# Performance work log

Measured on AMD Instinct MI355X. Metric: run time of the kernel, lower is better.

## Reference

```python
import jax, jax.numpy as jnp
import numpy as np

B, T, I, H, C = 2048, 1024, 6, 38, 8


def setup_inputs() -> dict:
    key = jax.random.key(0)
    ks = jax.random.split(key, 9)
    s = 1.0 / np.sqrt(H)  # PyTorch LSTM init scale
    return {
        "x": jax.random.normal(ks[0], (B, T, I), dtype=jnp.float32),
        "Wih0": jax.random.normal(ks[1], (4 * H, I), dtype=jnp.float32) * s,
        "Whh0": jax.random.normal(ks[2], (4 * H, H), dtype=jnp.float32) * s,
        "b0": jax.random.normal(ks[3], (4 * H,), dtype=jnp.float32) * s,
        "Wih1": jax.random.normal(ks[4], (4 * H, H), dtype=jnp.float32) * s,
        "Whh1": jax.random.normal(ks[5], (4 * H, H), dtype=jnp.float32) * s,
        "b1": jax.random.normal(ks[6], (4 * H,), dtype=jnp.float32) * s,
        "Wc": jax.random.normal(ks[7], (C, H), dtype=jnp.float32) * s,
        "bc": jax.random.normal(ks[8], (C,), dtype=jnp.float32) * s,
    }


def _lstm_layer(x, Wih, Whh, b):
    # x: [B, T, I]; PyTorch gate order: i, f, g, o; combined bias b = b_ih + b_hh
    Bsz = x.shape[0]
    Hh = Whh.shape[1]
    gx = jnp.einsum('bti,gi->btg', x, Wih) + b  # [B, T, 4H], input projection batched

    def step(carry, g_t):
        h, c = carry
        g = g_t + h @ Whh.T  # [B, 4H]
        i, f, gg, o = jnp.split(g, 4, axis=-1)
        i = jax.nn.sigmoid(i)
        f = jax.nn.sigmoid(f)
        gg = jnp.tanh(gg)
        o = jax.nn.sigmoid(o)
        c = f * c + i * gg
        h = o * jnp.tanh(c)
        return (h, c), h

    h0 = jnp.zeros((Bsz, Hh), dtype=x.dtype)
    c0 = jnp.zeros((Bsz, Hh), dtype=x.dtype)
    _, hs = jax.lax.scan(step, (h0, c0), jnp.swapaxes(gx, 0, 1))  # hs: [T, B, H]
    return jnp.swapaxes(hs, 0, 1)  # [B, T, H]


def reference(x, Wih0, Whh0, b0, Wih1, Whh1, b1, Wc, bc):
    # 2-layer LSTM (dropout is identity at inference), classify last timestep hidden
    h1 = _lstm_layer(x, Wih0, Whh0, b0)
    h2 = _lstm_layer(h1, Wih1, Whh1, b1)
    last = h2[:, -1, :]  # [B, H]
    return last @ Wc.T + bc  # [B, C]
```

## Files before the change

kernel.cpp:

```cpp
#include <hip/hip_runtime.h>

#define TT    1024
#define BATCH 2048
#define NI    6
#define NH    38
#define NG    152
#define NCLS  8
#define NB    8
#define BLK   640
#define KP1   68
#define KP2   100
#define XK    40
#define H2K   48

typedef _Float16 f16;
typedef _Float16 f16x4 __attribute__((ext_vector_type(4)));
typedef _Float16 f16x8 __attribute__((ext_vector_type(8)));
typedef float    f32x4 __attribute__((ext_vector_type(4)));

__device__ __forceinline__ float fsig(float v)  { return __fdividef(1.0f, 1.0f + __expf(-v)); }
__device__ __forceinline__ float ftanh(float v) { return 1.0f - __fdividef(2.0f, 1.0f + __expf(2.0f*v)); }

__device__ __forceinline__ float wget1(const float* Wih0, const float* Whh0, int r, int k) {
    if (r >= NG) return 0.0f;
    const int u = r >> 2, g = r & 3;
    if (k < NH) return Whh0[(size_t)(g*NH + u)*NH + k];
    if (k >= XK && k < XK + NI) return Wih0[(size_t)(g*NH + u)*NI + (k - XK)];
    return 0.0f;
}
__device__ __forceinline__ float wget2(const float* Wih1, const float* Whh1, int r, int k) {
    if (r >= NG) return 0.0f;
    const int u = r >> 2, g = r & 3;
    if (k < NH) return Wih1[(size_t)(g*NH + u)*NH + k];
    if (k >= H2K && k < H2K + NH) return Whh1[(size_t)(g*NH + u)*NH + (k - H2K)];
    return 0.0f;
}

__device__ __forceinline__ f16x8 ldA1(const float* Wih0, const float* Whh0,
                                      int Tg, int F, int m16, int qq) {
    f16x8 r;
    #pragma unroll
    for (int e = 0; e < 8; ++e) {
        const int kk = 32*F + ((e < 4) ? (qq*4 + e) : (16 + qq*4 + e - 4));
        r[e] = (f16)wget1(Wih0, Whh0, 16*Tg + m16, kk);
    }
    return r;
}
__device__ __forceinline__ f16x8 ldA2(const float* Wih1, const float* Whh1,
                                      int Tg, int F, int m16, int qq) {
    f16x8 r;
    #pragma unroll
    for (int e = 0; e < 8; ++e) {
        const int kk = 32*F + ((e < 4) ? (qq*4 + e) : (16 + qq*4 + e - 4));
        r[e] = (f16)wget2(Wih1, Whh1, 16*Tg + m16, kk);
    }
    return r;
}

__device__ __forceinline__ f16x8 ldB(const f16* rb, int off) {
    const f16x4 lo = *(const f16x4*)(rb + off);
    const f16x4 hi = *(const f16x4*)(rb + off + 16);
    f16x8 r;
    r[0]=lo[0]; r[1]=lo[1]; r[2]=lo[2]; r[3]=lo[3];
    r[4]=hi[0]; r[5]=hi[1]; r[6]=hi[2]; r[7]=hi[3];
    return r;
}

#define MFMA16(A, B, C) __builtin_amdgcn_mfma_f32_16x16x32_f16(A, B, C, 0, 0, 0)

#define PWCORE(A, CREG) \
    const float ig = fsig((A)[0] + bsv0), fg = fsig((A)[1] + bsv1); \
    const float gg = ftanh((A)[2] + bsv2), og = fsig((A)[3] + bsv3); \
    const float cc = fg * (CREG) + ig * gg; (CREG) = cc; \
    const f16 hv = (f16)(og * ftanh(cc));


__global__ __launch_bounds__(BLK, 1) void lstm2_kernel(
    const float* __restrict__ x,
    const float* __restrict__ Wih0, const float* __restrict__ Whh0, const float* __restrict__ b0,
    const float* __restrict__ Wih1, const float* __restrict__ Whh1, const float* __restrict__ b1,
    const float* __restrict__ Wc,   const float* __restrict__ bc,
    float* __restrict__ out)
{
    __shared__ __align__(16) f16 l1buf[2][16][KP1];
    __shared__ __align__(16) f16 l2buf[2][16][KP2];
    __shared__ float ldspad[19456];

    const int tid   = threadIdx.x;
    const int bbase = blockIdx.x * NB;
    const int wid   = tid >> 6, lane = tid & 63;
    const int n     = lane & 15, qq = lane >> 4;

    if (bc[0] > 3.0e38f) ldspad[tid] = x[tid];

    {
        int* p1 = (int*)&l1buf[0][0][0];
        for (int idx = tid; idx < 2*16*KP1/2; idx += BLK) p1[idx] = 0;
        int* p2 = (int*)&l2buf[0][0][0];
        for (int idx = tid; idx < 2*16*KP2/2; idx += BLK) p2[idx] = 0;
    }
    __syncthreads();
    if (tid < NB * NI) {
        const int b = tid / NI, j = tid % NI;
        l1buf[1][b][XK + j] = (f16)x[(size_t)(bbase + b)*TT*NI + j];
    }

    const bool isL1 = (wid < 5);
    const int  T0   = 2 * (isL1 ? wid : wid - 5);
    const int  u0   = 4*T0 + qq, u1 = u0 + 4;
    const bool wen0 = (u0 < NH) && (n < NB);
    const bool wen1 = (u1 < NH) && (n < NB);

    f16x8 w00, w01, w02, w10, w11, w12;
    float bs00=0.f,bs01=0.f,bs02=0.f,bs03=0.f, bs10=0.f,bs11=0.f,bs12=0.f,bs13=0.f;
    {
        f16x8 z8; 
        #pragma unroll
        for (int e = 0; e < 8; ++e) z8[e] = (f16)0;
        w02 = z8; w12 = z8;
        if (isL1) {
            w00 = ldA1(Wih0, Whh0, T0,   0, n, qq);
            w01 = ldA1(Wih0, Whh0, T0,   1, n, qq);
            w10 = ldA1(Wih0, Whh0, T0+1, 0, n, qq);
            w11 = ldA1(Wih0, Whh0, T0+1, 1, n, qq);
            if (u0 < NH) { bs00=b0[u0]; bs01=b0[NH+u0]; bs02=b0[2*NH+u0]; bs03=b0[3*NH+u0]; }
            if (u1 < NH) { bs10=b0[u1]; bs11=b0[NH+u1]; bs12=b0[2*NH+u1]; bs13=b0[3*NH+u1]; }
        } else {
            w00 = ldA2(Wih1, Whh1, T0,   0, n, qq);
            w01 = ldA2(Wih1, Whh1, T0,   1, n, qq);
            w02 = ldA2(Wih1, Whh1, T0,   2, n, qq);
            w10 = ldA2(Wih1, Whh1, T0+1, 0, n, qq);
            w11 = ldA2(Wih1, Whh1, T0+1, 1, n, qq);
            w12 = ldA2(Wih1, Whh1, T0+1, 2, n, qq);
            if (u0 < NH) { bs00=b1[u0]; bs01=b1[NH+u0]; bs02=b1[2*NH+u0]; bs03=b1[3*NH+u0]; }
            if (u1 < NH) { bs10=b1[u1]; bs11=b1[NH+u1]; bs12=b1[2*NH+u1]; bs13=b1[3*NH+u1]; }
        }
    }

    const bool isPF = (tid < NB * NI);
    const float* xptr = nullptr;
    f16 *pfw0 = nullptr, *pfw1 = nullptr;
    if (isPF) {
        const int b = tid / NI, j = tid % NI;
        xptr = x + (size_t)(bbase + b)*TT*NI + NI + j;
        pfw0 = &l1buf[0][b][XK + j];
        pfw1 = &l1buf[1][b][XK + j];
    }

    float c0 = 0.0f, c1 = 0.0f;

    __syncthreads();

    #pragma unroll 1
    for (int i = 0; i <= TT; ++i) {
        const int s = i & 1, rs = s ^ 1;

        float xv = 0.0f;
        const bool pf = isPF && (i + 1 < TT);
        if (pf) xv = *xptr;

        if (isL1) {
            if (i < TT) {
                const f16* rb = &l1buf[rs][n][0];
                const f16x8 B0 = ldB(rb, 4*qq);
                const f16x8 B1 = ldB(rb, 32 + 4*qq);
                f32x4 a0 = {0.f,0.f,0.f,0.f}, a1 = {0.f,0.f,0.f,0.f};
                a0 = MFMA16(w00, B0, a0);
                a0 = MFMA16(w01, B1, a0);
                a1 = MFMA16(w10, B0, a1);
                a1 = MFMA16(w11, B1, a1);
                {
                    const float bsv0=bs00, bsv1=bs01, bsv2=bs02, bsv3=bs03;
                    PWCORE(a0, c0)
                    if (wen0) { l1buf[s][n][u0] = hv; l2buf[s][n][u0] = hv; }
                }
                {
                    const float bsv0=bs10, bsv1=bs11, bsv2=bs12, bsv3=bs13;
                    PWCORE(a1, c1)
                    if (wen1) { l1buf[s][n][u1] = hv; l2buf[s][n][u1] = hv; }
                }
            }
        } else {
            if (i >= 1) {
                const f16* rb = &l2buf[rs][n][0];
                const f16x8 B0 = ldB(rb, 4*qq);
                const f16x8 B1 = ldB(rb, 32 + 4*qq);
                const f16x8 B2 = ldB(rb, 64 + 4*qq);
                f32x4 a0 = {0.f,0.f,0.f,0.f}, a1 = {0.f,0.f,0.f,0.f};
                a0 = MFMA16(w00, B0, a0);
                a0 = MFMA16(w01, B1, a0);
                a0 = MFMA16(w02, B2, a0);
                a1 = MFMA16(w10, B0, a1);
                a1 = MFMA16(w11, B1, a1);
                a1 = MFMA16(w12, B2, a1);
                {
                    const float bsv0=bs00, bsv1=bs01, bsv2=bs02, bsv3=bs03;
                    PWCORE(a0, c0)
                    if (wen0) l2buf[s][n][H2K + u0] = hv;
                }
                {
                    const float bsv0=bs10, bsv1=bs11, bsv2=bs12, bsv3=bs13;
                    PWCORE(a1, c1)
                    if (wen1) l2buf[s][n][H2K + u1] = hv;
                }
            }
        }

        if (pf) { *(s ? pfw1 : pfw0) = (f16)xv; xptr += NI; }
        __syncthreads();
    }

    if (tid < NB * NCLS) {
        const int b = tid >> 3, c = tid & 7;
        float a = bc[c];
        #pragma unroll
        for (int k = 0; k < NH; ++k)
            a += Wc[c*NH + k] * (float)l2buf[0][b][H2K + k];
        out[(size_t)(bbase + b)*NCLS + c] = a;
    }
    if (bc[0] > 3.0e38f) out[tid] = ldspad[BLK - tid];
}

extern "C" void kernel_launch(void* const* d_in, const int* in_sizes, int n_in,
                              void* d_out, int out_size, void* d_ws, size_t ws_size,
                              hipStream_t stream) {
    const float* x    = (const float*)d_in[0];
    const float* Wih0 = (const float*)d_in[1];
    const float* Whh0 = (const float*)d_in[2];
    const float* b0   = (const float*)d_in[3];
    const float* Wih1 = (const float*)d_in[4];
    const float* Whh1 = (const float*)d_in[5];
    const float* b1   = (const float*)d_in[6];
    const float* Wc   = (const float*)d_in[7];
    const float* bc   = (const float*)d_in[8];
    float* out = (float*)d_out;

    dim3 grid(BATCH / NB);
    dim3 block(BLK);
    hipLaunchKernelGGL(lstm2_kernel, grid, block, 0, stream,
                       x, Wih0, Whh0, b0, Wih1, Whh1, b1, Wc, bc, out);
}
```

Baseline: 1.277 ms.

## Unify LSTM layer buffers, batch x prefetch via LDS ring, use LDS-only barrier

Merges the layer-1 and layer-2 hidden-state buffers into one shared buffer, so layer-1 lanes write each hidden value once instead of twice. The per-step global load of x is replaced by a batched load of 8 timesteps into registers, which are staged through a 16-deep LDS ring. This lets the per-step barrier wait only on LDS counters (lgkmcnt) rather than on outstanding global loads. The risk is in ring and index timing: layer 2 now reads its input from the same slot layer 1 writes to, and the x ring must stay in sync with the double buffer.

```diff
diff --git a/kernel.cpp b/kernel.cpp
--- a/kernel.cpp
+++ b/kernel.cpp
@@ -8,10 +8,10 @@
 #define NCLS  8
 #define NB    8
 #define BLK   640
-#define KP1   68
-#define KP2   100
+#define UK    100
 #define XK    40
 #define H2K   48
+#define RD    16
 
 typedef _Float16 f16;
 typedef _Float16 f16x4 __attribute__((ext_vector_type(4)));
@@ -74,6 +74,11 @@
     const float cc = fg * (CREG) + ig * gg; (CREG) = cc; \
     const f16 hv = (f16)(og * ftanh(cc));
 
+#define LBAR() \
+    asm volatile("s_waitcnt lgkmcnt(0)" ::: "memory"); \
+    __builtin_amdgcn_s_barrier(); \
+    asm volatile("" ::: "memory"); \
+    __builtin_amdgcn_sched_barrier(0);
 
 __global__ __launch_bounds__(BLK, 1) void lstm2_kernel(
     const float* __restrict__ x,
@@ -82,9 +87,9 @@
     const float* __restrict__ Wc,   const float* __restrict__ bc,
     float* __restrict__ out)
 {
-    __shared__ __align__(16) f16 l1buf[2][16][KP1];
-    __shared__ __align__(16) f16 l2buf[2][16][KP2];
-    __shared__ float ldspad[19456];
+    __shared__ __align__(16) f16 ubuf[2][16][UK];
+    __shared__ __align__(16) f16 xring[RD][48];
+    __shared__ float ldspad[20160];
 
     const int tid   = threadIdx.x;
     const int bbase = blockIdx.x * NB;
@@ -94,16 +99,10 @@
     if (bc[0] > 3.0e38f) ldspad[tid] = x[tid];
 
     {
-        int* p1 = (int*)&l1buf[0][0][0];
-        for (int idx = tid; idx < 2*16*KP1/2; idx += BLK) p1[idx] = 0;
-        int* p2 = (int*)&l2buf[0][0][0];
-        for (int idx = tid; idx < 2*16*KP2/2; idx += BLK) p2[idx] = 0;
+        int* p = (int*)&ubuf[0][0][0];
+        for (int idx = tid; idx < 2*16*UK/2; idx += BLK) p[idx] = 0;
     }
     __syncthreads();
-    if (tid < NB * NI) {
-        const int b = tid / NI, j = tid % NI;
-        l1buf[1][b][XK + j] = (f16)x[(size_t)(bbase + b)*TT*NI + j];
-    }
 
     const bool isL1 = (wid < 5);
     const int  T0   = 2 * (isL1 ? wid : wid - 5);
@@ -114,7 +113,7 @@
     f16x8 w00, w01, w02, w10, w11, w12;
     float bs00=0.f,bs01=0.f,bs02=0.f,bs03=0.f, bs10=0.f,bs11=0.f,bs12=0.f,bs13=0.f;
     {
-        f16x8 z8; 
+        f16x8 z8;
         #pragma unroll
         for (int e = 0; e < 8; ++e) z8[e] = (f16)0;
         w02 = z8; w12 = z8;
@@ -137,14 +136,28 @@
         }
     }
 
+    const f16* rowp0 = &ubuf[0][n][0];
+    const f16* rowp1 = &ubuf[1][n][0];
+    f16 *wpA0, *wpA1, *wpB0, *wpB1;
+    if (isL1) {
+        wpA0 = &ubuf[0][n][u0];       wpA1 = &ubuf[1][n][u0];
+        wpB0 = &ubuf[0][n][u1];       wpB1 = &ubuf[1][n][u1];
+    } else {
+        wpA0 = &ubuf[0][n][H2K+u0];   wpA1 = &ubuf[1][n][H2K+u0];
+        wpB0 = &ubuf[0][n][H2K+u1];   wpB1 = &ubuf[1][n][H2K+u1];
+    }
+
     const bool isPF = (tid < NB * NI);
-    const float* xptr = nullptr;
-    f16 *pfw0 = nullptr, *pfw1 = nullptr;
+    const int  pb = tid / NI, pj = tid % NI;
+    const float* xgbase = x + (size_t)(bbase + pb)*TT*NI + pj;
+    f16* ringl = &xring[0][pb*NI + pj];
+    f16 *pwx0 = &ubuf[0][pb][XK + pj], *pwx1 = &ubuf[1][pb][XK + pj];
+    float pl0=0.f,pl1=0.f,pl2=0.f,pl3=0.f,pl4=0.f,pl5=0.f,pl6=0.f,pl7=0.f;
+
     if (isPF) {
-        const int b = tid / NI, j = tid % NI;
-        xptr = x + (size_t)(bbase + b)*TT*NI + NI + j;
-        pfw0 = &l1buf[0][b][XK + j];
-        pfw1 = &l1buf[1][b][XK + j];
+        *pwx1 = (f16)xgbase[0];
+        #pragma unroll
+        for (int t = 1; t <= 7; ++t) ringl[t*48] = (f16)xgbase[(size_t)t*NI];
     }
 
     float c0 = 0.0f, c1 = 0.0f;
@@ -153,15 +166,23 @@
 
     #pragma unroll 1
     for (int i = 0; i <= TT; ++i) {
-        const int s = i & 1, rs = s ^ 1;
-
-        float xv = 0.0f;
-        const bool pf = isPF && (i + 1 < TT);
-        if (pf) xv = *xptr;
+        const int s = i & 1;
+
+        if (isPF && (i & 7) == 0) {
+            const int tb = i + 8;
+            pl0 = (tb+0 < TT) ? xgbase[(size_t)(tb+0)*NI] : 0.f;
+            pl1 = (tb+1 < TT) ? xgbase[(size_t)(tb+1)*NI] : 0.f;
+            pl2 = (tb+2 < TT) ? xgbase[(size_t)(tb+2)*NI] : 0.f;
+            pl3 = (tb+3 < TT) ? xgbase[(size_t)(tb+3)*NI] : 0.f;
+            pl4 = (tb+4 < TT) ? xgbase[(size_t)(tb+4)*NI] : 0.f;
+            pl5 = (tb+5 < TT) ? xgbase[(size_t)(tb+5)*NI] : 0.f;
+            pl6 = (tb+6 < TT) ? xgbase[(size_t)(tb+6)*NI] : 0.f;
+            pl7 = (tb+7 < TT) ? xgbase[(size_t)(tb+7)*NI] : 0.f;
+        }
 
         if (isL1) {
             if (i < TT) {
-                const f16* rb = &l1buf[rs][n][0];
+                const f16* rb = s ? rowp0 : rowp1;
                 const f16x8 B0 = ldB(rb, 4*qq);
                 const f16x8 B1 = ldB(rb, 32 + 4*qq);
                 f32x4 a0 = {0.f,0.f,0.f,0.f}, a1 = {0.f,0.f,0.f,0.f};
@@ -172,17 +193,17 @@
                 {
                     const float bsv0=bs00, bsv1=bs01, bsv2=bs02, bsv3=bs03;
                     PWCORE(a0, c0)
-                    if (wen0) { l1buf[s][n][u0] = hv; l2buf[s][n][u0] = hv; }
+                    if (wen0) *(s ? wpA1 : wpA0) = hv;
                 }
                 {
                     const float bsv0=bs10, bsv1=bs11, bsv2=bs12, bsv3=bs13;
                     PWCORE(a1, c1)
-                    if (wen1) { l1buf[s][n][u1] = hv; l2buf[s][n][u1] = hv; }
+                    if (wen1) *(s ? wpB1 : wpB0) = hv;
                 }
             }
         } else {
             if (i >= 1) {
-                const f16* rb = &l2buf[rs][n][0];
+                const f16* rb = s ? rowp0 : rowp1;
                 const f16x8 B0 = ldB(rb, 4*qq);
                 const f16x8 B1 = ldB(rb, 32 + 4*qq);
                 const f16x8 B2 = ldB(rb, 64 + 4*qq);
@@ -196,18 +217,35 @@
                 {
                     const float bsv0=bs00, bsv1=bs01, bsv2=bs02, bsv3=bs03;
                     PWCORE(a0, c0)
-                    if (wen0) l2buf[s][n][H2K + u0] = hv;
+                    if (wen0) *(s ? wpA1 : wpA0) = hv;
                 }
                 {
                     const float bsv0=bs10, bsv1=bs11, bsv2=bs12, bsv3=bs13;
                     PWCORE(a1, c1)
-                    if (wen1) l2buf[s][n][H2K + u1] = hv;
-                }
-            }
-        }
-
-        if (pf) { *(s ? pfw1 : pfw0) = (f16)xv; xptr += NI; }
-        __syncthreads();
+                    if (wen1) *(s ? wpB1 : wpB0) = hv;
+                }
+            }
+        }
+
+        if (isPF) {
+            if (i + 1 < TT) {
+                const f16 xv = ringl[((i + 1) & (RD-1)) * 48];
+                *(s ? pwx1 : pwx0) = xv;
+            }
+            if ((i & 7) == 6) {
+                const int tb = i + 2;
+                ringl[((tb+0)&(RD-1))*48] = (f16)pl0;
+                ringl[((tb+1)&(RD-1))*48] = (f16)pl1;
+                ringl[((tb+2)&(RD-1))*48] = (f16)pl2;
+                ringl[((tb+3)&(RD-1))*48] = (f16)pl3;
+                ringl[((tb+4)&(RD-1))*48] = (f16)pl4;
+                ringl[((tb+5)&(RD-1))*48] = (f16)pl5;
+                ringl[((tb+6)&(RD-1))*48] = (f16)pl6;
+                ringl[((tb+7)&(RD-1))*48] = (f16)pl7;
+            }
+        }
+
+        LBAR()
     }
 
     if (tid < NB * NCLS) {
@@ -215,7 +253,7 @@
         float a = bc[c];
         #pragma unroll
         for (int k = 0; k < NH; ++k)
-            a += Wc[c*NH + k] * (float)l2buf[0][b][H2K + k];
+            a += Wc[c*NH + k] * (float)ubuf[0][b][H2K + k];
         out[(size_t)(bbase + b)*NCLS + c] = a;
     }
     if (bc[0] > 3.0e38f) out[tid] = ldspad[BLK - tid];
```

Measured after the change: 1.290 ms. No clear change (+1.1%).
